# Kernel tuning notes

Hardware: AMD Instinct MI355X
Metric: run time of the kernel (lower is better)

## Reference

```python
import jax, jax.numpy as jnp
import numpy as np

N_NODES = 50000
N_EDGES = 640000
IN_DIM = 128
OUT_DIM = 128
EDGE_DIM = 16
N_HEADS = 4
HEAD_DIM = OUT_DIM // N_HEADS  # 32
LN_EPS = 1e-5


def setup_inputs() -> dict:
    key = jax.random.key(0)
    ks = jax.random.split(key, 6)
    h = jax.random.normal(ks[0], (N_NODES, IN_DIM), dtype=jnp.float32)
    edge_index = jax.random.randint(ks[1], (2, N_EDGES), 0, N_NODES, dtype=jnp.int64)
    edge_feat = jax.random.normal(ks[2], (N_EDGES, EDGE_DIM), dtype=jnp.float32)
    # parameters (xavier-ish scaling)
    W = jax.random.normal(ks[3], (OUT_DIM, IN_DIM), dtype=jnp.float32) * (1.0 / np.sqrt(IN_DIM))
    W_e = jax.random.normal(ks[4], (N_HEADS, EDGE_DIM), dtype=jnp.float32) * (1.0 / np.sqrt(EDGE_DIM))
    a = jax.random.normal(ks[5], (N_HEADS, 2 * HEAD_DIM), dtype=jnp.float32) * (1.0 / np.sqrt(2 * HEAD_DIM))
    ln_scale = jnp.ones((OUT_DIM,), dtype=jnp.float32)
    ln_bias = jnp.zeros((OUT_DIM,), dtype=jnp.float32)
    return {"h": h, "edge_index": edge_index, "edge_feat": edge_feat,
            "W": W, "W_e": W_e, "a": a, "ln_scale": ln_scale, "ln_bias": ln_bias}


def _layer_norm(x, scale, bias):
    mu = jnp.mean(x, axis=-1, keepdims=True)
    var = jnp.mean(jnp.square(x - mu), axis=-1, keepdims=True)
    return (x - mu) * jax.lax.rsqrt(var + LN_EPS) * scale + bias


def reference(h, edge_index, edge_feat, W, W_e, a, ln_scale, ln_bias):
    N = h.shape[0]
    H, D = N_HEADS, HEAD_DIM
    src, dst = edge_index[0], edge_index[1]

    Wh = (h @ W.T).reshape(N, H, D)                       # [N,H,D]
    Wh_src = Wh[src]                                       # [E,H,D] gather
    Wh_dst = Wh[dst]                                       # [E,H,D] gather
    # e_ij = leaky_relu(a . [Wh_src || Wh_dst]) + W_e . edge_feat
    attn = (jnp.concatenate([Wh_src, Wh_dst], axis=-1) * a[None]).sum(-1)  # [E,H]
    attn = jax.nn.leaky_relu(attn, negative_slope=0.2)
    attn = attn + edge_feat @ W_e.T                        # [E,H]

    # scatter-softmax over incoming edges per destination node
    max_v = jax.ops.segment_max(attn, dst, num_segments=N)   # [N,H]
    max_v = jnp.maximum(max_v, -1e9)                         # match torch init
    exp_v = jnp.exp(attn - max_v[dst])                       # [E,H]
    denom = jax.ops.segment_sum(exp_v, dst, num_segments=N)  # [N,H]
    alpha = exp_v / (denom[dst] + 1e-9)                      # [E,H]

    # per-head scatter-add aggregation: h_i' = sum_j alpha_ij * Wh_j
    agg = jax.ops.segment_sum(alpha[..., None] * Wh_src, dst, num_segments=N)  # [N,H,D]
    out = agg.reshape(N, H * D)
    return _layer_norm(jax.nn.gelu(out, approximate=False), ln_scale, ln_bias)
```

## Files before the change

### kernel.cpp

```cpp
#include <hip/hip_runtime.h>
#include <math.h>

#define N_NODES 50000
#define N_EDGES 640000
#define DIM 128
#define EDGE_DIM 16
#define N_HEADS 4
#define HEAD_DIM 32
#define CAPB 48

typedef __attribute__((ext_vector_type(8))) short bf16x8;
typedef __attribute__((ext_vector_type(4))) float floatx4;

__device__ __forceinline__ unsigned short f2bf(float f) {
    unsigned int x = __float_as_uint(f);
    return (unsigned short)((x + 0x7FFFu + ((x >> 16) & 1u)) >> 16);
}
__device__ __forceinline__ float bf2f(unsigned short u) {
    return __uint_as_float(((unsigned int)u) << 16);
}
__device__ __forceinline__ float bfu2f_lo(unsigned int u) {
    return __uint_as_float(u << 16);
}
__device__ __forceinline__ float bfu2f_hi(unsigned int u) {
    return __uint_as_float(u & 0xFFFF0000u);
}

__global__ __launch_bounds__(256) void k_gemm(
    const float* __restrict__ h,
    const float* __restrict__ W,
    const float* __restrict__ a,
    unsigned short* __restrict__ Whbf,
    float* __restrict__ sc,
    int* __restrict__ counts)
{
    __shared__ unsigned short w_lds[16 * 128 * 8];
    __shared__ unsigned short p_lds[16 * 16 * 8];
    int t = threadIdx.x;

    if (t < 64) {
        int ci = blockIdx.x * 64 + t;
        if (ci < N_NODES) counts[ci] = 0;
    }

    {
        int r = t >> 1, halfc = t & 1;
        const float* wr = W + (size_t)r * DIM + halfc * 64;
#pragma unroll
        for (int j = 0; j < 8; ++j) {
            float4 x0 = *(const float4*)(wr + j * 8);
            float4 x1 = *(const float4*)(wr + j * 8 + 4);
            bf16x8 f;
            f[0] = (short)f2bf(x0.x); f[1] = (short)f2bf(x0.y);
            f[2] = (short)f2bf(x0.z); f[3] = (short)f2bf(x0.w);
            f[4] = (short)f2bf(x1.x); f[5] = (short)f2bf(x1.y);
            f[6] = (short)f2bf(x1.z); f[7] = (short)f2bf(x1.w);
            int ch = halfc * 8 + j;
            *(bf16x8*)&w_lds[(ch * 128 + r) * 8] = f;
        }
    }
    {
        unsigned int* p32 = (unsigned int*)p_lds;
        int ch = t >> 4, sub = t & 15;
        p32[ch * 64 + 32 + sub] = 0;
        p32[ch * 64 + 48 + sub] = 0;
    }
    __syncthreads();

    if (t < 128) {
        int j = t & 7, cg = t >> 3;
        int hh = j & 3, off = (j >> 2) * 32;
        int rot = t & 7;
        float dot[8] = {0.f, 0.f, 0.f, 0.f, 0.f, 0.f, 0.f, 0.f};
        for (int dd = 0; dd < 32; ++dd) {
            int d = (dd + rot) & 31;
            bf16x8 wv = *(const bf16x8*)&w_lds[(cg * 128 + hh * 32 + d) * 8];
            float av = a[hh * 64 + off + d];
#pragma unroll
            for (int k = 0; k < 8; ++k)
                dot[k] += bf2f((unsigned short)wv[k]) * av;
        }
        bf16x8 pf;
#pragma unroll
        for (int k = 0; k < 8; ++k) pf[k] = (short)f2bf(dot[k]);
        *(bf16x8*)&p_lds[(cg * 16 + j) * 8] = pf;
    }
    __syncthreads();

    int wave = t >> 6, lane = t & 63;
    int nb = blockIdx.x * 64 + wave * 16;
    int m = lane & 15, q = lane >> 4;
    int node = nb + m;
    bool nvalid = node < N_NODES;

    bf16x8 hfrag[4];
#pragma unroll
    for (int kt = 0; kt < 4; ++kt) {
        bf16x8 f;
        if (nvalid) {
            const float* p = h + (size_t)node * DIM + kt * 32 + q * 8;
            float4 x0 = *(const float4*)(p);
            float4 x1 = *(const float4*)(p + 4);
            f[0] = (short)f2bf(x0.x); f[1] = (short)f2bf(x0.y);
            f[2] = (short)f2bf(x0.z); f[3] = (short)f2bf(x0.w);
            f[4] = (short)f2bf(x1.x); f[5] = (short)f2bf(x1.y);
            f[6] = (short)f2bf(x1.z); f[7] = (short)f2bf(x1.w);
        } else {
#pragma unroll
            for (int j = 0; j < 8; ++j) f[j] = 0;
        }
        hfrag[kt] = f;
    }

    floatx4 accS = {0.f, 0.f, 0.f, 0.f};
#pragma unroll
    for (int kt = 0; kt < 4; ++kt) {
        bf16x8 pfrag = *(const bf16x8*)&p_lds[((kt * 4 + q) * 16 + m) * 8];
        accS = __builtin_amdgcn_mfma_f32_16x16x32_bf16(pfrag, hfrag[kt], accS, 0, 0, 0);
    }
    if (q < 2 && nvalid) {
        *(float4*)(sc + (size_t)node * 8 + q * 4) =
            make_float4(accS[0], accS[1], accS[2], accS[3]);
    }

#pragma unroll
    for (int dt = 0; dt < 8; ++dt) {
        floatx4 acc = {0.f, 0.f, 0.f, 0.f};
#pragma unroll
        for (int kt = 0; kt < 4; ++kt) {
            bf16x8 wfrag = *(const bf16x8*)&w_lds[((kt * 4 + q) * 128 + dt * 16 + m) * 8];
            acc = __builtin_amdgcn_mfma_f32_16x16x32_bf16(wfrag, hfrag[kt], acc, 0, 0, 0);
        }
        if (nvalid) {
            unsigned int lo = ((unsigned int)f2bf(acc[1]) << 16) | f2bf(acc[0]);
            unsigned int hi = ((unsigned int)f2bf(acc[3]) << 16) | f2bf(acc[2]);
            uint2 pk; pk.x = lo; pk.y = hi;
            *(uint2*)(Whbf + (size_t)node * DIM + dt * 16 + q * 4) = pk;
        }
    }
}

__global__ __launch_bounds__(256) void k_scatter(
    const int* __restrict__ ei,
    const float* __restrict__ ef,
    const float* __restrict__ We,
    const float* __restrict__ sc,
    int* __restrict__ counts,
    uint4* __restrict__ brec)
{
    __shared__ float ef_s[256 * 17];
    int t = threadIdx.x;
    int e0 = blockIdx.x * 256;

    const float4* g = (const float4*)(ef + (size_t)e0 * 16);
#pragma unroll
    for (int i = 0; i < 4; ++i) {
        int gidx = i * 256 + t;
        float4 v = g[gidx];
        float* d = ef_s + (gidx >> 2) * 17 + (gidx & 3) * 4;
        d[0] = v.x; d[1] = v.y; d[2] = v.z; d[3] = v.w;
    }
    __syncthreads();

    int e = e0 + t;
    int src = ei[e], dst = ei[N_EDGES + e];
    float4 ss = *(const float4*)(sc + (size_t)src * 8);
    float4 sd = *(const float4*)(sc + (size_t)dst * 8 + 4);
    float lg[4] = {ss.x + sd.x, ss.y + sd.y, ss.z + sd.z, ss.w + sd.w};

    const float* fr = ef_s + t * 17;
#pragma unroll
    for (int hh = 0; hh < 4; ++hh) {
        const float4* wep = (const float4*)(We + hh * 16);
        float4 w0 = wep[0], w1 = wep[1], w2 = wep[2], w3 = wep[3];
        float ed = fr[0]  * w0.x + fr[1]  * w0.y + fr[2]  * w0.z + fr[3]  * w0.w
                 + fr[4]  * w1.x + fr[5]  * w1.y + fr[6]  * w1.z + fr[7]  * w1.w
                 + fr[8]  * w2.x + fr[9]  * w2.y + fr[10] * w2.z + fr[11] * w2.w
                 + fr[12] * w3.x + fr[13] * w3.y + fr[14] * w3.z + fr[15] * w3.w;
        float s = lg[hh];
        s = s > 0.f ? s : 0.2f * s;
        lg[hh] = __expf(s + ed);
    }
    int slot = atomicAdd(counts + dst, 1);
    if (slot < CAPB) {
        uint4 rec;
        rec.x = (unsigned int)src;
        rec.y = ((unsigned int)f2bf(lg[1]) << 16) | f2bf(lg[0]);
        rec.z = ((unsigned int)f2bf(lg[3]) << 16) | f2bf(lg[2]);
        rec.w = 0;
        brec[(size_t)dst * CAPB + slot] = rec;
    }
}

__global__ __launch_bounds__(256) void k_node(
    const int* __restrict__ counts,
    const uint4* __restrict__ brec,
    const unsigned short* __restrict__ Whbf,
    const float* __restrict__ ln_scale, const float* __restrict__ ln_bias,
    float* __restrict__ out)
{
    __shared__ __align__(16) float p_s[2][CAPB * 4];
    __shared__ int s_s[2][CAPB];
    __shared__ float comb[2][64][3];
    int w = threadIdx.x >> 6, l = threadIdx.x & 63;
    int nw = w >> 1, half = w & 1;
    int n = blockIdx.x * 2 + nw;
    int deg = counts[n];
    deg = deg < CAPB ? deg : CAPB;
    size_t base = (size_t)n * CAPB;

    if (l < 24) {
        int slot = half * 24 + l;
        uint4 rec = make_uint4(0u, 0u, 0u, 0u);
        if (slot < deg) rec = brec[base + slot];
        float4 pv;
        pv.x = bfu2f_lo(rec.y); pv.y = bfu2f_hi(rec.y);
        pv.z = bfu2f_lo(rec.z); pv.w = bfu2f_hi(rec.z);
        *(float4*)&p_s[nw][slot * 4] = pv;
        s_s[nw][slot] = (int)rec.x;
    }
    __syncthreads();

    int hb = l >> 4;
    float den = 0.f, a0 = 0.f, a1 = 0.f;
    int nch = (deg + 7) >> 3;
    for (int c = half; c < nch; c += 2) {
        int e0 = c * 8;
        float pv[8];
        unsigned int uu[8];
#pragma unroll
        for (int j = 0; j < 8; ++j) {
            int e = e0 + j;
            int src = s_s[nw][e];
            pv[j] = p_s[nw][e * 4 + hb];
            uu[j] = *(const unsigned int*)(Whbf + (size_t)src * DIM + 2 * l);
        }
#pragma unroll
        for (int j = 0; j < 8; ++j) {
            den += pv[j];
            a0 += pv[j] * bfu2f_lo(uu[j]);
            a1 += pv[j] * bfu2f_hi(uu[j]);
        }
    }
    if (half == 1) {
        comb[nw][l][0] = den;
        comb[nw][l][1] = a0;
        comb[nw][l][2] = a1;
    }
    __syncthreads();
    if (half == 1) return;

    den += comb[nw][l][0];
    a0  += comb[nw][l][1];
    a1  += comb[nw][l][2];

    float dd = den + 1e-9f;
    float x0 = a0 / dd, x1 = a1 / dd;
    float g0 = 0.5f * x0 * (1.f + erff(x0 * 0.70710678118654752f));
    float g1 = 0.5f * x1 * (1.f + erff(x1 * 0.70710678118654752f));
    float s = g0 + g1, ss = g0 * g0 + g1 * g1;
#pragma unroll
    for (int off = 1; off < 64; off <<= 1) {
        s += __shfl_xor(s, off, 64);
        ss += __shfl_xor(ss, off, 64);
    }
    float mu = s * (1.f / 128.f);
    float var = ss * (1.f / 128.f) - mu * mu;
    float rstd = rsqrtf(var + 1e-5f);
    float2 sca = *(const float2*)(ln_scale + 2 * l);
    float2 bi = *(const float2*)(ln_bias + 2 * l);
    float2 o;
    o.x = (g0 - mu) * rstd * sca.x + bi.x;
    o.y = (g1 - mu) * rstd * sca.y + bi.y;
    *(float2*)(out + (size_t)n * DIM + 2 * l) = o;
}

extern "C" void kernel_launch(void* const* d_in, const int* in_sizes, int n_in,
                              void* d_out, int out_size, void* d_ws, size_t ws_size,
                              hipStream_t stream) {
    const float* h   = (const float*)d_in[0];
    const int*   ei  = (const int*)d_in[1];
    const float* ef  = (const float*)d_in[2];
    const float* W   = (const float*)d_in[3];
    const float* We  = (const float*)d_in[4];
    const float* a   = (const float*)d_in[5];
    const float* lsc = (const float*)d_in[6];
    const float* lbi = (const float*)d_in[7];

    char* ws = (char*)d_ws;
    size_t off = 0;
    unsigned short* Whbf = (unsigned short*)(ws + off); off += (size_t)N_NODES * DIM * 2;
    float* sc    = (float*)(ws + off); off += (size_t)N_NODES * 8 * 4;
    int*   counts= (int*)(ws + off);   off += (size_t)N_NODES * 4;
    uint4* brec  = (uint4*)(ws + off); off += (size_t)N_NODES * CAPB * 16;

    k_gemm<<<(N_NODES + 63) / 64, 256, 0, stream>>>(h, W, a, Whbf, sc, counts);
    k_scatter<<<N_EDGES / 256, 256, 0, stream>>>(ei, ef, We, sc, counts, brec);
    k_node<<<N_NODES / 2, 256, 0, stream>>>(counts, brec, Whbf, lsc, lbi,
                                            (float*)d_out);
}
```

Before: 205.0 us.

## Use one wave per node with half-wave edge split; hoist scatter loads and atomic

The node kernel now assigns one 64-lane wavefront per destination node instead of two. Each half-wave handles alternate edges and loads 8-byte bf16 vectors, and the halves combine through a cross-lane shuffle rather than shared memory and a second barrier. This removes the shared-memory combine step and lets each block process four nodes. The scatter kernel issues the edge-feature loads, index loads, atomicAdd and score gathers before the LDS staging, so their latency overlaps. In exchange, half the lanes sit idle at the output store and each lane holds more registers.

```diff
diff --git a/kernel.cpp b/kernel.cpp
--- a/kernel.cpp
+++ b/kernel.cpp
@@ -153,21 +153,24 @@
     int e0 = blockIdx.x * 256;
 
     const float4* g = (const float4*)(ef + (size_t)e0 * 16);
+    float4 v0 = g[t], v1 = g[256 + t], v2 = g[512 + t], v3 = g[768 + t];
+
+    int e = e0 + t;
+    int src = ei[e], dst = ei[N_EDGES + e];
+    int slot = atomicAdd(counts + dst, 1);
+    float4 ss = *(const float4*)(sc + (size_t)src * 8);
+    float4 sd = *(const float4*)(sc + (size_t)dst * 8 + 4);
+
+    float4 vv[4] = {v0, v1, v2, v3};
 #pragma unroll
     for (int i = 0; i < 4; ++i) {
         int gidx = i * 256 + t;
-        float4 v = g[gidx];
         float* d = ef_s + (gidx >> 2) * 17 + (gidx & 3) * 4;
-        d[0] = v.x; d[1] = v.y; d[2] = v.z; d[3] = v.w;
+        d[0] = vv[i].x; d[1] = vv[i].y; d[2] = vv[i].z; d[3] = vv[i].w;
     }
     __syncthreads();
 
-    int e = e0 + t;
-    int src = ei[e], dst = ei[N_EDGES + e];
-    float4 ss = *(const float4*)(sc + (size_t)src * 8);
-    float4 sd = *(const float4*)(sc + (size_t)dst * 8 + 4);
     float lg[4] = {ss.x + sd.x, ss.y + sd.y, ss.z + sd.z, ss.w + sd.w};
-
     const float* fr = ef_s + t * 17;
 #pragma unroll
     for (int hh = 0; hh < 4; ++hh) {
@@ -181,7 +184,6 @@
         s = s > 0.f ? s : 0.2f * s;
         lg[hh] = __expf(s + ed);
     }
-    int slot = atomicAdd(counts + dst, 1);
     if (slot < CAPB) {
         uint4 rec;
         rec.x = (unsigned int)src;
@@ -199,80 +201,82 @@
     const float* __restrict__ ln_scale, const float* __restrict__ ln_bias,
     float* __restrict__ out)
 {
-    __shared__ __align__(16) float p_s[2][CAPB * 4];
-    __shared__ int s_s[2][CAPB];
-    __shared__ float comb[2][64][3];
+    __shared__ __align__(16) float p_s[4][CAPB * 4];
+    __shared__ int s_s[4][CAPB];
     int w = threadIdx.x >> 6, l = threadIdx.x & 63;
-    int nw = w >> 1, half = w & 1;
-    int n = blockIdx.x * 2 + nw;
+    int n = blockIdx.x * 4 + w;
     int deg = counts[n];
     deg = deg < CAPB ? deg : CAPB;
     size_t base = (size_t)n * CAPB;
 
-    if (l < 24) {
-        int slot = half * 24 + l;
+    if (l < CAPB) {
         uint4 rec = make_uint4(0u, 0u, 0u, 0u);
-        if (slot < deg) rec = brec[base + slot];
+        if (l < deg) rec = brec[base + l];
         float4 pv;
         pv.x = bfu2f_lo(rec.y); pv.y = bfu2f_hi(rec.y);
         pv.z = bfu2f_lo(rec.z); pv.w = bfu2f_hi(rec.z);
-        *(float4*)&p_s[nw][slot * 4] = pv;
-        s_s[nw][slot] = (int)rec.x;
+        *(float4*)&p_s[w][l * 4] = pv;
+        s_s[w][l] = (int)rec.x;
     }
     __syncthreads();
 
-    int hb = l >> 4;
-    float den = 0.f, a0 = 0.f, a1 = 0.f;
-    int nch = (deg + 7) >> 3;
-    for (int c = half; c < nch; c += 2) {
-        int e0 = c * 8;
+    int li = l & 31, half = l >> 5;
+    int hb = li >> 3;
+    float den = 0.f, b0 = 0.f, b1 = 0.f, b2 = 0.f, b3 = 0.f;
+    int nch = (deg + 15) >> 4;
+    for (int c = 0; c < nch; ++c) {
+        int e0 = c * 16 + half;
         float pv[8];
-        unsigned int uu[8];
+        uint2 uu[8];
 #pragma unroll
         for (int j = 0; j < 8; ++j) {
-            int e = e0 + j;
-            int src = s_s[nw][e];
-            pv[j] = p_s[nw][e * 4 + hb];
-            uu[j] = *(const unsigned int*)(Whbf + (size_t)src * DIM + 2 * l);
+            int e = e0 + j * 2;
+            int src = s_s[w][e];
+            pv[j] = p_s[w][e * 4 + hb];
+            uu[j] = *(const uint2*)(Whbf + (size_t)src * DIM + li * 4);
         }
 #pragma unroll
         for (int j = 0; j < 8; ++j) {
             den += pv[j];
-            a0 += pv[j] * bfu2f_lo(uu[j]);
-            a1 += pv[j] * bfu2f_hi(uu[j]);
-        }
-    }
-    if (half == 1) {
-        comb[nw][l][0] = den;
-        comb[nw][l][1] = a0;
-        comb[nw][l][2] = a1;
-    }
-    __syncthreads();
-    if (half == 1) return;
-
-    den += comb[nw][l][0];
-    a0  += comb[nw][l][1];
-    a1  += comb[nw][l][2];
+            b0 += pv[j] * bfu2f_lo(uu[j].x);
+            b1 += pv[j] * bfu2f_hi(uu[j].x);
+            b2 += pv[j] * bfu2f_lo(uu[j].y);
+            b3 += pv[j] * bfu2f_hi(uu[j].y);
+        }
+    }
+    den += __shfl_xor(den, 32, 64);
+    b0 += __shfl_xor(b0, 32, 64);
+    b1 += __shfl_xor(b1, 32, 64);
+    b2 += __shfl_xor(b2, 32, 64);
+    b3 += __shfl_xor(b3, 32, 64);
 
     float dd = den + 1e-9f;
-    float x0 = a0 / dd, x1 = a1 / dd;
-    float g0 = 0.5f * x0 * (1.f + erff(x0 * 0.70710678118654752f));
-    float g1 = 0.5f * x1 * (1.f + erff(x1 * 0.70710678118654752f));
-    float s = g0 + g1, ss = g0 * g0 + g1 * g1;
-#pragma unroll
-    for (int off = 1; off < 64; off <<= 1) {
+    float x0 = b0 / dd, x1 = b1 / dd, x2 = b2 / dd, x3 = b3 / dd;
+    const float k = 0.70710678118654752f;
+    float g0 = 0.5f * x0 * (1.f + erff(x0 * k));
+    float g1 = 0.5f * x1 * (1.f + erff(x1 * k));
+    float g2 = 0.5f * x2 * (1.f + erff(x2 * k));
+    float g3 = 0.5f * x3 * (1.f + erff(x3 * k));
+    float s = g0 + g1 + g2 + g3;
+    float ss = g0 * g0 + g1 * g1 + g2 * g2 + g3 * g3;
+#pragma unroll
+    for (int off = 1; off <= 16; off <<= 1) {
         s += __shfl_xor(s, off, 64);
         ss += __shfl_xor(ss, off, 64);
     }
     float mu = s * (1.f / 128.f);
     float var = ss * (1.f / 128.f) - mu * mu;
     float rstd = rsqrtf(var + 1e-5f);
-    float2 sca = *(const float2*)(ln_scale + 2 * l);
-    float2 bi = *(const float2*)(ln_bias + 2 * l);
-    float2 o;
-    o.x = (g0 - mu) * rstd * sca.x + bi.x;
-    o.y = (g1 - mu) * rstd * sca.y + bi.y;
-    *(float2*)(out + (size_t)n * DIM + 2 * l) = o;
+    if (half == 0) {
+        float4 sca = *(const float4*)(ln_scale + li * 4);
+        float4 bi = *(const float4*)(ln_bias + li * 4);
+        float4 o;
+        o.x = (g0 - mu) * rstd * sca.x + bi.x;
+        o.y = (g1 - mu) * rstd * sca.y + bi.y;
+        o.z = (g2 - mu) * rstd * sca.z + bi.z;
+        o.w = (g3 - mu) * rstd * sca.w + bi.w;
+        *(float4*)(out + (size_t)n * DIM + li * 4) = o;
+    }
 }
 
 extern "C" void kernel_launch(void* const* d_in, const int* in_sizes, int n_in,
@@ -296,6 +300,6 @@
 
     k_gemm<<<(N_NODES + 63) / 64, 256, 0, stream>>>(h, W, a, Whbf, sc, counts);
     k_scatter<<<N_EDGES / 256, 256, 0, stream>>>(ei, ef, We, sc, counts, brec);
-    k_node<<<N_NODES / 2, 256, 0, stream>>>(counts, brec, Whbf, lsc, lbi,
+    k_node<<<N_NODES / 4, 256, 0, stream>>>(counts, brec, Whbf, lsc, lbi,
                                             (float*)d_out);
 }
```

Result: faster. 197.1 us (-3.9%).
